# Performance work log

Measured on AMD Instinct MI355X. Metric: run time of the kernel, lower is better.

Reference implementation:

```python
import jax, jax.numpy as jnp
import numpy as np
import math

B, T, C, NH = 4, 2048, 1024, 16
D = C // NH  # 64, rotary_dim == D

def _rope_tables():
    inv_freq = 1.0 / (10000.0 ** (np.arange(0, D, 2, dtype=np.float32) / D))
    t = np.arange(T, dtype=np.float32)
    freqs = np.outer(t, inv_freq)                 # [T, D/2]
    emb = np.concatenate([freqs, freqs], axis=-1)  # [T, D]
    return jnp.asarray(np.cos(emb))[None], jnp.asarray(np.sin(emb))[None]  # [1,T,D]

def setup_inputs() -> dict:
    key = jax.random.key(0)
    ks = jax.random.split(key, 3)
    x = jax.random.normal(ks[0], (B, T, C), dtype=jnp.float32)
    w_attn = jax.random.normal(ks[1], (3 * C, C), dtype=jnp.float32) * (1.0 / math.sqrt(C))
    b_attn = jnp.zeros((3 * C,), dtype=jnp.float32)
    w_proj = jax.random.normal(ks[2], (C, C), dtype=jnp.float32) * (1.0 / math.sqrt(C))
    b_proj = jnp.zeros((C,), dtype=jnp.float32)
    cos, sin = _rope_tables()
    return {"x": x, "w_attn": w_attn, "b_attn": b_attn,
            "w_proj": w_proj, "b_proj": b_proj, "cos": cos, "sin": sin}

def _rotate_half(u):
    u1, u2 = jnp.split(u, 2, axis=-1)
    return jnp.concatenate([-u2, u1], axis=-1)

def reference(x, w_attn, b_attn, w_proj, b_proj, cos, sin):
    Bx, Tx, Cx = x.shape
    nh, d = NH, Cx // NH
    # fused QKV projection (torch Linear: y = x @ W^T + b)
    qkv = x @ w_attn.T + b_attn                      # [B,T,3C]
    q, k, v = jnp.split(qkv, 3, axis=-1)
    q = q.reshape(Bx, Tx, nh, d).transpose(0, 2, 1, 3)  # [B,nh,T,d]
    k = k.reshape(Bx, Tx, nh, d).transpose(0, 2, 1, 3)
    v = v.reshape(Bx, Tx, nh, d).transpose(0, 2, 1, 3)
    # RoPE (rotary_dim == d, full head)
    c = cos[:, None, :, :]  # [1,1,T,d]
    s = sin[:, None, :, :]
    q = q * c + _rotate_half(q) * s
    k = k * c + _rotate_half(k) * s
    # naive causal attention
    scores = jnp.einsum("bhqd,bhkd->bhqk", q, k) / math.sqrt(d)
    causal = jnp.tril(jnp.ones((Tx, Tx), dtype=bool))
    scores = jnp.where(causal[None, None], scores, -jnp.inf)
    att = jax.nn.softmax(scores, axis=-1)
    y = jnp.einsum("bhqk,bhkd->bhqd", att, v)        # [B,nh,T,d]
    y = y.transpose(0, 2, 1, 3).reshape(Bx, Tx, Cx)
    return y @ w_proj.T + b_proj
```

## Files before the change

### kernel.cpp

```cpp
#include <hip/hip_runtime.h>

typedef __bf16 bf16_t;
typedef bf16_t bf16x8 __attribute__((ext_vector_type(8)));
typedef bf16_t bf16x4 __attribute__((ext_vector_type(4)));
typedef float f32x4 __attribute__((ext_vector_type(4)));

constexpr int BATCH = 4, SEQ = 2048, CH = 1024, NHEAD = 16, HD = 64;
constexpr int BM = 128, BN = 128, BKK = 32;

#define LGKM_FENCE() __asm__ __volatile__("s_waitcnt lgkmcnt(0)" ::: "memory")
#define VM_FENCE() __asm__ __volatile__("s_waitcnt vmcnt(0)" ::: "memory")

__device__ __forceinline__ void g2lds16(const bf16_t* g, bf16_t* l) {
  __builtin_amdgcn_global_load_lds((__attribute__((address_space(1))) void*)(g),
                                   (__attribute__((address_space(3))) void*)(l),
                                   16, 0, 0);
}

__device__ __forceinline__ f32x4 mfma16(bf16x8 a, bf16x8 b, f32x4 c) {
  return __builtin_amdgcn_mfma_f32_16x16x32_bf16(a, b, c, 0, 0, 0);
}

__global__ __launch_bounds__(256) void cvt_kernel(const float4* __restrict__ src,
                                                  ushort4* __restrict__ dst, int n4) {
  int i = blockIdx.x * 256 + threadIdx.x;
  if (i >= n4) return;
  float4 f = src[i];
  ushort4 o;
  o.x = __builtin_bit_cast(unsigned short, (bf16_t)f.x);
  o.y = __builtin_bit_cast(unsigned short, (bf16_t)f.y);
  o.z = __builtin_bit_cast(unsigned short, (bf16_t)f.z);
  o.w = __builtin_bit_cast(unsigned short, (bf16_t)f.w);
  dst[i] = o;
}

__device__ __forceinline__ void gemm_mainloop(const bf16_t* __restrict__ A,
                                              const bf16_t* __restrict__ W, int Kdim,
                                              int m0, int n0,
                                              bf16_t* As, bf16_t* Bs,
                                              f32x4 acc[4][4]) {
  const int tid = threadIdx.x;
  const int lane = tid & 63, w = tid >> 6;
  const int quad = lane >> 4, l16 = lane & 15;
  const int wm = (w >> 1) << 6, wn = (w & 1) << 6;
  const int srow = (w << 5) + (lane >> 2);
  const int scol = (lane & 3) << 3;
  const bf16_t* ga0 = A + (size_t)(m0 + srow) * Kdim + scol;
  const bf16_t* ga1 = A + (size_t)(m0 + srow + 16) * Kdim + scol;
  const bf16_t* gb0 = W + (size_t)(n0 + srow) * Kdim + scol;
  const bf16_t* gb1 = W + (size_t)(n0 + srow + 16) * Kdim + scol;
  bf16_t* la0 = As + srow * BKK + scol;
  bf16_t* la1 = As + (srow + 16) * BKK + scol;
  bf16_t* lb0 = Bs + srow * BKK + scol;
  bf16_t* lb1 = Bs + (srow + 16) * BKK + scol;
  for (int k0 = 0; k0 < Kdim; k0 += BKK) {
    g2lds16(ga0 + k0, la0);
    g2lds16(ga1 + k0, la1);
    g2lds16(gb0 + k0, lb0);
    g2lds16(gb1 + k0, lb1);
    VM_FENCE();
    __syncthreads();
    bf16x8 av[4], bv[4];
#pragma unroll
    for (int i = 0; i < 4; i++)
      av[i] = *(const bf16x8*)&As[(wm + i * 16 + l16) * BKK + quad * 8];
#pragma unroll
    for (int i = 0; i < 4; i++)
      bv[i] = *(const bf16x8*)&Bs[(wn + i * 16 + l16) * BKK + quad * 8];
#pragma unroll
    for (int mi = 0; mi < 4; mi++)
#pragma unroll
      for (int ni = 0; ni < 4; ni++)
        acc[mi][ni] = mfma16(av[mi], bv[ni], acc[mi][ni]);
    __syncthreads();
  }
}

__global__ __launch_bounds__(256) void qkv_rope_kernel(
    const bf16_t* __restrict__ X, const bf16_t* __restrict__ Wa,
    const float* __restrict__ ba, const float* __restrict__ cosT,
    const float* __restrict__ sinT, bf16_t* __restrict__ Q,
    bf16_t* __restrict__ Ko, bf16_t* __restrict__ VT) {
  constexpr int TSTRIDE = 68;
  __shared__ __align__(16) char smem[4 * 64 * TSTRIDE * 2];
  bf16_t* As = (bf16_t*)smem;
  bf16_t* Bs = As + BM * BKK;

  f32x4 acc[4][4];
#pragma unroll
  for (int i = 0; i < 4; i++)
#pragma unroll
    for (int j = 0; j < 4; j++) acc[i][j] = (f32x4){0.f, 0.f, 0.f, 0.f};

  const int n0 = blockIdx.x * BN, m0 = blockIdx.y * BM;
  gemm_mainloop(X, Wa, CH, m0, n0, As, Bs, acc);

  const int tid = threadIdx.x, lane = tid & 63, w = tid >> 6;
  const int quad = lane >> 4, l16 = lane & 15;
  const int wm = (w >> 1) << 6, wn = (w & 1) << 6;
  const int nbase = n0 + wn;
  const int part = nbase >> 10;
  const int h = (nbase & 1023) >> 6;
  const int mbase = m0 + wm;
  const int bb = mbase >> 11;
  const size_t headbase = ((size_t)(bb * NHEAD + h)) * SEQ * HD;

  if (part < 2) {
    bf16_t* O = (part == 0) ? Q : Ko;
#pragma unroll
    for (int mi = 0; mi < 4; mi++)
#pragma unroll
      for (int r = 0; r < 4; r++) {
        int m = mbase + mi * 16 + quad * 4 + r;
        int t = m & (SEQ - 1);
        const float* cr = cosT + t * HD;
        const float* sr = sinT + t * HD;
        size_t rowo = headbase + (size_t)t * HD;
#pragma unroll
        for (int ni = 0; ni < 2; ni++) {
          int d0 = ni * 16 + l16, d1 = d0 + 32;
          float v0 = acc[mi][ni][r] + ba[nbase + d0];
          float v1 = acc[mi][ni + 2][r] + ba[nbase + d1];
          float r0 = v0 * cr[d0] - v1 * sr[d0];
          float r1 = v1 * cr[d1] + v0 * sr[d1];
          O[rowo + d0] = (bf16_t)r0;
          O[rowo + d1] = (bf16_t)r1;
        }
      }
  } else {
    bf16_t* tb = (bf16_t*)smem + w * 64 * TSTRIDE;
    int t0 = mbase & (SEQ - 1);
#pragma unroll
    for (int mi = 0; mi < 4; mi++)
#pragma unroll
      for (int ni = 0; ni < 4; ni++) {
        int d = ni * 16 + l16;
        float bias = ba[nbase + d];
#pragma unroll
        for (int r = 0; r < 4; r++) {
          float v = acc[mi][ni][r] + bias;
          tb[d * TSTRIDE + mi * 16 + quad * 4 + r] = (bf16_t)v;
        }
      }
    LGKM_FENCE();
    int half = lane >> 5, l5 = lane & 31;
    size_t vbase = ((size_t)(bb * NHEAD + h)) * HD * SEQ;
#pragma unroll
    for (int it = 0; it < 32; it++) {
      int d = it * 2 + half;
      unsigned int val = *(const unsigned int*)&tb[d * TSTRIDE + l5 * 2];
      *(unsigned int*)&VT[vbase + (size_t)d * SEQ + t0 + l5 * 2] = val;
    }
  }
}

constexpr int PS = 80;
constexpr float SCL = 0.125f * 1.44269504089f;

__device__ __forceinline__ void sm_update(f32x4 (&s)[4], float& mr, float& lr,
                                          f32x4 (&y)[4], bf16_t* Prow,
                                          bool domask, int lim) {
  if (domask) {
#pragma unroll
    for (int ni = 0; ni < 4; ni++)
#pragma unroll
      for (int r = 0; r < 4; r++)
        if (ni * 16 + r > lim) s[ni][r] = -1e30f;
  }
  f32x4 mx;
#pragma unroll
  for (int r = 0; r < 4; r++)
    mx[r] = fmaxf(fmaxf(s[0][r], s[1][r]), fmaxf(s[2][r], s[3][r]));
  float cm = fmaxf(fmaxf(mx[0], mx[1]), fmaxf(mx[2], mx[3]));
  cm = fmaxf(cm, __shfl_xor(cm, 16));
  cm = fmaxf(cm, __shfl_xor(cm, 32));
  float mn = fmaxf(mr, cm);
  float hof = -SCL * mn;
  float al = __builtin_exp2f(fmaf(mr, SCL, hof));
  mr = mn;
  float sum = 0.f;
#pragma unroll
  for (int ni = 0; ni < 4; ni++) {
    float p0 = __builtin_exp2f(fmaf(s[ni][0], SCL, hof));
    float p1 = __builtin_exp2f(fmaf(s[ni][1], SCL, hof));
    float p2 = __builtin_exp2f(fmaf(s[ni][2], SCL, hof));
    float p3 = __builtin_exp2f(fmaf(s[ni][3], SCL, hof));
    bf16x4 pk = {(bf16_t)p0, (bf16_t)p1, (bf16_t)p2, (bf16_t)p3};
    *(bf16x4*)&Prow[ni * 16] = pk;
    sum += (p0 + p1) + (p2 + p3);
  }
  lr = fmaf(lr, al, sum);
#pragma unroll
  for (int ni = 0; ni < 4; ni++) y[ni] *= al;
}

__global__ __launch_bounds__(256) void flash_kernel(const bf16_t* __restrict__ Q,
                                                    const bf16_t* __restrict__ Kg,
                                                    const bf16_t* __restrict__ VT,
                                                    bf16_t* __restrict__ att) {
  __shared__ __align__(16) bf16_t Ks[2][64 * 64];
  __shared__ __align__(16) bf16_t Vs[2][64 * 64];
  __shared__ __align__(16) bf16_t Pt[8][16 * PS];
  const int tid = threadIdx.x, w = tid >> 6, lane = tid & 63;
  const int quad = lane >> 4, l16 = lane & 15;
  const int bh = blockIdx.y;
  const bf16_t* Qp = Q + (size_t)bh * SEQ * HD;
  const bf16_t* Kb = Kg + (size_t)bh * SEQ * HD;
  const bf16_t* Vb = VT + (size_t)bh * HD * SEQ;
  const int grow = lane >> 3;
  const int gj8 = ((lane & 7) ^ grow) * 8;
  const int i0 = w * 2;
  const int sw = l16 & 7;
  const int bloc = bh >> 4, hh = bh & 15;
  bf16_t* PA = &Pt[w * 2 + 0][l16 * PS + quad * 4];
  bf16_t* PB = &Pt[w * 2 + 1][l16 * PS + quad * 4];
  const bf16_t* PAr = &Pt[w * 2 + 0][l16 * PS + quad * 8];
  const bf16_t* PBr = &Pt[w * 2 + 1][l16 * PS + quad * 8];

  auto stage = [&](int kcs, int b) {
#pragma unroll
    for (int ii = 0; ii < 2; ii++) {
      int i = i0 + ii;
      g2lds16(Kb + (size_t)(kcs + i * 8 + grow) * HD + gj8, &Ks[b][(i * 64 + lane) * 8]);
      g2lds16(Vb + (size_t)(i * 8 + grow) * SEQ + kcs + gj8, &Vs[b][(i * 64 + lane) * 8]);
    }
  };

  for (int sp = 0; sp < 2; ++sp) {
    const int qb = sp ? (int)blockIdx.x : 15 - (int)blockIdx.x;
    const int q0 = qb * 128;
    const int mA = q0 + w * 16, mB = mA + 64;
    bf16x8 aqA0 = *(const bf16x8*)&Qp[(size_t)(mA + l16) * HD + quad * 8];
    bf16x8 aqA1 = *(const bf16x8*)&Qp[(size_t)(mA + l16) * HD + 32 + quad * 8];
    bf16x8 aqB0 = *(const bf16x8*)&Qp[(size_t)(mB + l16) * HD + quad * 8];
    bf16x8 aqB1 = *(const bf16x8*)&Qp[(size_t)(mB + l16) * HD + 32 + quad * 8];
    float mrA = -1e30f, lrA = 0.f, mrB = -1e30f, lrB = 0.f;
    f32x4 yA[4], yB[4];
#pragma unroll
    for (int ni = 0; ni < 4; ni++) {
      yA[ni] = (f32x4){0.f, 0.f, 0.f, 0.f};
      yB[ni] = (f32x4){0.f, 0.f, 0.f, 0.f};
    }
    const int nch = 2 * qb + 2;

    stage(0, 0);
    VM_FENCE();
    __syncthreads();

    for (int c = 0; c < nch; ++c) {
      const int kc = c * 64, buf = c & 1;
      if (c + 1 < nch) stage(kc + 64, buf ^ 1);
      const bool doA = (c + 1 < nch);
      f32x4 sA[4], sB[4];
#pragma unroll
      for (int ni = 0; ni < 4; ni++) {
        bf16x8 k0 = *(const bf16x8*)&Ks[buf][((ni * 16 + l16) * 8 + (quad ^ sw)) * 8];
        bf16x8 k1 = *(const bf16x8*)&Ks[buf][((ni * 16 + l16) * 8 + ((4 + quad) ^ sw)) * 8];
        f32x4 z = (f32x4){0.f, 0.f, 0.f, 0.f};
        sB[ni] = mfma16(k1, aqB1, mfma16(k0, aqB0, z));
        if (doA) sA[ni] = mfma16(k1, aqA1, mfma16(k0, aqA0, z));
      }
      sm_update(sB, mrB, lrB, yB, PB, c == nch - 1, mB + l16 - kc - quad * 4);
      if (doA)
        sm_update(sA, mrA, lrA, yA, PA, c == nch - 2, mA + l16 - kc - quad * 4);
      LGKM_FENCE();
      bf16x8 pB0 = *(const bf16x8*)&PBr[0];
      bf16x8 pB1 = *(const bf16x8*)&PBr[32];
      bf16x8 pA0, pA1;
      if (doA) {
        pA0 = *(const bf16x8*)&PAr[0];
        pA1 = *(const bf16x8*)&PAr[32];
      }
#pragma unroll
      for (int ni = 0; ni < 4; ni++) {
        bf16x8 v0 = *(const bf16x8*)&Vs[buf][((ni * 16 + l16) * 8 + (quad ^ sw)) * 8];
        bf16x8 v1 = *(const bf16x8*)&Vs[buf][((ni * 16 + l16) * 8 + ((4 + quad) ^ sw)) * 8];
        yB[ni] = mfma16(v1, pB1, mfma16(v0, pB0, yB[ni]));
        if (doA) yA[ni] = mfma16(v1, pA1, mfma16(v0, pA0, yA[ni]));
      }
      VM_FENCE();
      __syncthreads();
    }

    lrA += __shfl_xor(lrA, 16);
    lrA += __shfl_xor(lrA, 32);
    lrB += __shfl_xor(lrB, 16);
    lrB += __shfl_xor(lrB, 32);
    float invA = 1.f / lrA, invB = 1.f / lrB;
    size_t rbA = ((size_t)bloc * SEQ + mA + l16) * CH + hh * HD + quad * 4;
    size_t rbB = ((size_t)bloc * SEQ + mB + l16) * CH + hh * HD + quad * 4;
#pragma unroll
    for (int ni = 0; ni < 4; ni++) {
      bf16x4 oA = {(bf16_t)(yA[ni][0] * invA), (bf16_t)(yA[ni][1] * invA),
                   (bf16_t)(yA[ni][2] * invA), (bf16_t)(yA[ni][3] * invA)};
      bf16x4 oB = {(bf16_t)(yB[ni][0] * invB), (bf16_t)(yB[ni][1] * invB),
                   (bf16_t)(yB[ni][2] * invB), (bf16_t)(yB[ni][3] * invB)};
      *(bf16x4*)&att[rbA + ni * 16] = oA;
      *(bf16x4*)&att[rbB + ni * 16] = oB;
    }
  }
}

__global__ __launch_bounds__(256) void proj_kernel(const bf16_t* __restrict__ A,
                                                   const bf16_t* __restrict__ Wp,
                                                   const float* __restrict__ bp,
                                                   float* __restrict__ out) {
  __shared__ __align__(16) bf16_t As[BM * BKK];
  __shared__ __align__(16) bf16_t Bs[BN * BKK];
  f32x4 acc[4][4];
#pragma unroll
  for (int i = 0; i < 4; i++)
#pragma unroll
    for (int j = 0; j < 4; j++) acc[i][j] = (f32x4){0.f, 0.f, 0.f, 0.f};
  const int n0 = blockIdx.x * BN, m0 = blockIdx.y * BM;
  gemm_mainloop(A, Wp, CH, m0, n0, As, Bs, acc);
  const int tid = threadIdx.x, lane = tid & 63, w = tid >> 6;
  const int quad = lane >> 4, l16 = lane & 15;
  const int wm = (w >> 1) << 6, wn = (w & 1) << 6;
  const int nbase = n0 + wn, mbase = m0 + wm;
#pragma unroll
  for (int mi = 0; mi < 4; mi++)
#pragma unroll
    for (int r = 0; r < 4; r++) {
      int m = mbase + mi * 16 + quad * 4 + r;
#pragma unroll
      for (int ni = 0; ni < 4; ni++) {
        int n = nbase + ni * 16 + l16;
        out[(size_t)m * CH + n] = acc[mi][ni][r] + bp[n];
      }
    }
}

extern "C" void kernel_launch(void* const* d_in, const int* in_sizes, int n_in,
                              void* d_out, int out_size, void* d_ws, size_t ws_size,
                              hipStream_t stream) {
  const float* x      = (const float*)d_in[0];
  const float* w_attn = (const float*)d_in[1];
  const float* b_attn = (const float*)d_in[2];
  const float* w_proj = (const float*)d_in[3];
  const float* b_proj = (const float*)d_in[4];
  const float* cosT   = (const float*)d_in[5];
  const float* sinT   = (const float*)d_in[6];
  float* out = (float*)d_out;

  bf16_t* xbf  = (bf16_t*)d_ws;
  bf16_t* wabf = xbf + (size_t)8192 * 1024;
  bf16_t* wpbf = wabf + (size_t)3072 * 1024;
  bf16_t* Qb   = wpbf + (size_t)1024 * 1024;
  bf16_t* Kb   = Qb + (size_t)8388608;
  bf16_t* VTb  = Kb + (size_t)8388608;
  bf16_t* attb = VTb + (size_t)8388608;

  cvt_kernel<<<8192, 256, 0, stream>>>((const float4*)x, (ushort4*)xbf, 2097152);
  cvt_kernel<<<3072, 256, 0, stream>>>((const float4*)w_attn, (ushort4*)wabf, 786432);
  cvt_kernel<<<1024, 256, 0, stream>>>((const float4*)w_proj, (ushort4*)wpbf, 262144);
  qkv_rope_kernel<<<dim3(24, 64), 256, 0, stream>>>(xbf, wabf, b_attn, cosT, sinT,
                                                    Qb, Kb, VTb);
  flash_kernel<<<dim3(8, 64), 256, 0, stream>>>(Qb, Kb, VTb, attb);
  proj_kernel<<<dim3(8, 64), 256, 0, stream>>>(attb, wpbf, b_proj, out);
}
```

Before: 310.7 us.

## Restructure flash attention grid, fold softmax scale into Q, lazy rescale

Folds the softmax scale and log2e factor into Q inside the QKV/RoPE epilogue, so the flash kernel computes exp2(s - m) directly. Online-softmax rescaling of the accumulator is skipped when no row max grows in the wave. The flash grid changes from 8x64 blocks that each process two query blocks to 1024 one-dimensional blocks, one query block each, ordered heaviest-first. The P staging buffer shrinks to one XOR-swizzled tile per wave with occupancy hinted at 4 blocks/CU, and V fragments are preloaded and reused by both row halves. Risks are more blocks with uneven causal work and the extra precision loss from rounding the pre-scaled Q to bf16.

```diff
diff --git a/kernel.cpp b/kernel.cpp
--- a/kernel.cpp
+++ b/kernel.cpp
@@ -10,6 +10,7 @@
 
 #define LGKM_FENCE() __asm__ __volatile__("s_waitcnt lgkmcnt(0)" ::: "memory")
 #define VM_FENCE() __asm__ __volatile__("s_waitcnt vmcnt(0)" ::: "memory")
+#define REORDER_FENCE() __asm__ __volatile__("" ::: "memory")
 
 __device__ __forceinline__ void g2lds16(const bf16_t* g, bf16_t* l) {
   __builtin_amdgcn_global_load_lds((__attribute__((address_space(1))) void*)(g),
@@ -76,6 +77,8 @@
   }
 }
 
+constexpr float SCL = 0.125f * 1.44269504089f;
+
 __global__ __launch_bounds__(256) void qkv_rope_kernel(
     const bf16_t* __restrict__ X, const bf16_t* __restrict__ Wa,
     const float* __restrict__ ba, const float* __restrict__ cosT,
@@ -107,6 +110,7 @@
 
   if (part < 2) {
     bf16_t* O = (part == 0) ? Q : Ko;
+    const float post = (part == 0) ? SCL : 1.0f;
 #pragma unroll
     for (int mi = 0; mi < 4; mi++)
 #pragma unroll
@@ -121,8 +125,8 @@
           int d0 = ni * 16 + l16, d1 = d0 + 32;
           float v0 = acc[mi][ni][r] + ba[nbase + d0];
           float v1 = acc[mi][ni + 2][r] + ba[nbase + d1];
-          float r0 = v0 * cr[d0] - v1 * sr[d0];
-          float r1 = v1 * cr[d1] + v0 * sr[d1];
+          float r0 = (v0 * cr[d0] - v1 * sr[d0]) * post;
+          float r1 = (v1 * cr[d1] + v0 * sr[d1]) * post;
           O[rowo + d0] = (bf16_t)r0;
           O[rowo + d1] = (bf16_t)r1;
         }
@@ -154,11 +158,8 @@
   }
 }
 
-constexpr int PS = 80;
-constexpr float SCL = 0.125f * 1.44269504089f;
-
 __device__ __forceinline__ void sm_update(f32x4 (&s)[4], float& mr, float& lr,
-                                          f32x4 (&y)[4], bf16_t* Prow,
+                                          f32x4 (&y)[4], bf16_t* Prow, int xk,
                                           bool domask, int lim) {
   if (domask) {
 #pragma unroll
@@ -174,36 +175,39 @@
   float cm = fmaxf(fmaxf(mx[0], mx[1]), fmaxf(mx[2], mx[3]));
   cm = fmaxf(cm, __shfl_xor(cm, 16));
   cm = fmaxf(cm, __shfl_xor(cm, 32));
-  float mn = fmaxf(mr, cm);
-  float hof = -SCL * mn;
-  float al = __builtin_exp2f(fmaf(mr, SCL, hof));
-  mr = mn;
+  if (__any(cm > mr)) {
+    float mn = fmaxf(mr, cm);
+    float al = __builtin_exp2f(mr - mn);
+    mr = mn;
+    lr *= al;
+#pragma unroll
+    for (int ni = 0; ni < 4; ni++) y[ni] *= al;
+  }
   float sum = 0.f;
 #pragma unroll
   for (int ni = 0; ni < 4; ni++) {
-    float p0 = __builtin_exp2f(fmaf(s[ni][0], SCL, hof));
-    float p1 = __builtin_exp2f(fmaf(s[ni][1], SCL, hof));
-    float p2 = __builtin_exp2f(fmaf(s[ni][2], SCL, hof));
-    float p3 = __builtin_exp2f(fmaf(s[ni][3], SCL, hof));
+    float p0 = __builtin_exp2f(s[ni][0] - mr);
+    float p1 = __builtin_exp2f(s[ni][1] - mr);
+    float p2 = __builtin_exp2f(s[ni][2] - mr);
+    float p3 = __builtin_exp2f(s[ni][3] - mr);
     bf16x4 pk = {(bf16_t)p0, (bf16_t)p1, (bf16_t)p2, (bf16_t)p3};
-    *(bf16x4*)&Prow[ni * 16] = pk;
+    *(bf16x4*)&Prow[((ni ^ xk) << 4)] = pk;
     sum += (p0 + p1) + (p2 + p3);
   }
-  lr = fmaf(lr, al, sum);
-#pragma unroll
-  for (int ni = 0; ni < 4; ni++) y[ni] *= al;
-}
-
-__global__ __launch_bounds__(256) void flash_kernel(const bf16_t* __restrict__ Q,
-                                                    const bf16_t* __restrict__ Kg,
-                                                    const bf16_t* __restrict__ VT,
-                                                    bf16_t* __restrict__ att) {
+  lr += sum;
+}
+
+__global__ __launch_bounds__(256, 4) void flash_kernel(const bf16_t* __restrict__ Q,
+                                                       const bf16_t* __restrict__ Kg,
+                                                       const bf16_t* __restrict__ VT,
+                                                       bf16_t* __restrict__ att) {
   __shared__ __align__(16) bf16_t Ks[2][64 * 64];
   __shared__ __align__(16) bf16_t Vs[2][64 * 64];
-  __shared__ __align__(16) bf16_t Pt[8][16 * PS];
+  __shared__ __align__(16) bf16_t Pt[4][16 * 64];
   const int tid = threadIdx.x, w = tid >> 6, lane = tid & 63;
   const int quad = lane >> 4, l16 = lane & 15;
-  const int bh = blockIdx.y;
+  const int qb = 15 - ((int)blockIdx.x >> 6);
+  const int bh = (int)blockIdx.x & 63;
   const bf16_t* Qp = Q + (size_t)bh * SEQ * HD;
   const bf16_t* Kb = Kg + (size_t)bh * SEQ * HD;
   const bf16_t* Vb = VT + (size_t)bh * HD * SEQ;
@@ -211,11 +215,12 @@
   const int gj8 = ((lane & 7) ^ grow) * 8;
   const int i0 = w * 2;
   const int sw = l16 & 7;
+  const int xk = l16 & 3;
   const int bloc = bh >> 4, hh = bh & 15;
-  bf16_t* PA = &Pt[w * 2 + 0][l16 * PS + quad * 4];
-  bf16_t* PB = &Pt[w * 2 + 1][l16 * PS + quad * 4];
-  const bf16_t* PAr = &Pt[w * 2 + 0][l16 * PS + quad * 8];
-  const bf16_t* PBr = &Pt[w * 2 + 1][l16 * PS + quad * 8];
+  bf16_t* Pw = &Pt[w][l16 * 64];
+  bf16_t* Pwr = Pw + quad * 4;
+  const int rs0 = ((2 * quad) ^ (xk << 2)) << 2;
+  const int rs1 = ((8 + 2 * quad) ^ (xk << 2)) << 2;
 
   auto stage = [&](int kcs, int b) {
 #pragma unroll
@@ -226,78 +231,77 @@
     }
   };
 
-  for (int sp = 0; sp < 2; ++sp) {
-    const int qb = sp ? (int)blockIdx.x : 15 - (int)blockIdx.x;
-    const int q0 = qb * 128;
-    const int mA = q0 + w * 16, mB = mA + 64;
-    bf16x8 aqA0 = *(const bf16x8*)&Qp[(size_t)(mA + l16) * HD + quad * 8];
-    bf16x8 aqA1 = *(const bf16x8*)&Qp[(size_t)(mA + l16) * HD + 32 + quad * 8];
-    bf16x8 aqB0 = *(const bf16x8*)&Qp[(size_t)(mB + l16) * HD + quad * 8];
-    bf16x8 aqB1 = *(const bf16x8*)&Qp[(size_t)(mB + l16) * HD + 32 + quad * 8];
-    float mrA = -1e30f, lrA = 0.f, mrB = -1e30f, lrB = 0.f;
-    f32x4 yA[4], yB[4];
+  const int q0 = qb * 128;
+  const int mA = q0 + w * 16, mB = mA + 64;
+  bf16x8 aqA0 = *(const bf16x8*)&Qp[(size_t)(mA + l16) * HD + quad * 8];
+  bf16x8 aqA1 = *(const bf16x8*)&Qp[(size_t)(mA + l16) * HD + 32 + quad * 8];
+  bf16x8 aqB0 = *(const bf16x8*)&Qp[(size_t)(mB + l16) * HD + quad * 8];
+  bf16x8 aqB1 = *(const bf16x8*)&Qp[(size_t)(mB + l16) * HD + 32 + quad * 8];
+  float mrA = -1e30f, lrA = 0.f, mrB = -1e30f, lrB = 0.f;
+  f32x4 yA[4], yB[4];
+#pragma unroll
+  for (int ni = 0; ni < 4; ni++) {
+    yA[ni] = (f32x4){0.f, 0.f, 0.f, 0.f};
+    yB[ni] = (f32x4){0.f, 0.f, 0.f, 0.f};
+  }
+  const int nch = 2 * qb + 2;
+
+  stage(0, 0);
+  VM_FENCE();
+  __syncthreads();
+
+  for (int c = 0; c < nch; ++c) {
+    const int kc = c * 64, buf = c & 1;
+    if (c + 1 < nch) stage(kc + 64, buf ^ 1);
+    const bool doA = (c + 1 < nch);
+    f32x4 sA[4], sB[4];
+    bf16x8 vf0[4], vf1[4];
 #pragma unroll
     for (int ni = 0; ni < 4; ni++) {
-      yA[ni] = (f32x4){0.f, 0.f, 0.f, 0.f};
-      yB[ni] = (f32x4){0.f, 0.f, 0.f, 0.f};
-    }
-    const int nch = 2 * qb + 2;
-
-    stage(0, 0);
+      bf16x8 k0 = *(const bf16x8*)&Ks[buf][((ni * 16 + l16) * 8 + (quad ^ sw)) * 8];
+      bf16x8 k1 = *(const bf16x8*)&Ks[buf][((ni * 16 + l16) * 8 + ((4 + quad) ^ sw)) * 8];
+      f32x4 z = (f32x4){0.f, 0.f, 0.f, 0.f};
+      sB[ni] = mfma16(k1, aqB1, mfma16(k0, aqB0, z));
+      if (doA) sA[ni] = mfma16(k1, aqA1, mfma16(k0, aqA0, z));
+      vf0[ni] = *(const bf16x8*)&Vs[buf][((ni * 16 + l16) * 8 + (quad ^ sw)) * 8];
+      vf1[ni] = *(const bf16x8*)&Vs[buf][((ni * 16 + l16) * 8 + ((4 + quad) ^ sw)) * 8];
+    }
+    sm_update(sB, mrB, lrB, yB, Pwr, xk, c == nch - 1, mB + l16 - kc - quad * 4);
+    LGKM_FENCE();
+    bf16x8 pB0 = *(const bf16x8*)&Pw[rs0];
+    bf16x8 pB1 = *(const bf16x8*)&Pw[rs1];
+#pragma unroll
+    for (int ni = 0; ni < 4; ni++)
+      yB[ni] = mfma16(vf1[ni], pB1, mfma16(vf0[ni], pB0, yB[ni]));
+    if (doA) {
+      REORDER_FENCE();
+      sm_update(sA, mrA, lrA, yA, Pwr, xk, c == nch - 2, mA + l16 - kc - quad * 4);
+      LGKM_FENCE();
+      bf16x8 pA0 = *(const bf16x8*)&Pw[rs0];
+      bf16x8 pA1 = *(const bf16x8*)&Pw[rs1];
+#pragma unroll
+      for (int ni = 0; ni < 4; ni++)
+        yA[ni] = mfma16(vf1[ni], pA1, mfma16(vf0[ni], pA0, yA[ni]));
+    }
     VM_FENCE();
     __syncthreads();
-
-    for (int c = 0; c < nch; ++c) {
-      const int kc = c * 64, buf = c & 1;
-      if (c + 1 < nch) stage(kc + 64, buf ^ 1);
-      const bool doA = (c + 1 < nch);
-      f32x4 sA[4], sB[4];
-#pragma unroll
-      for (int ni = 0; ni < 4; ni++) {
-        bf16x8 k0 = *(const bf16x8*)&Ks[buf][((ni * 16 + l16) * 8 + (quad ^ sw)) * 8];
-        bf16x8 k1 = *(const bf16x8*)&Ks[buf][((ni * 16 + l16) * 8 + ((4 + quad) ^ sw)) * 8];
-        f32x4 z = (f32x4){0.f, 0.f, 0.f, 0.f};
-        sB[ni] = mfma16(k1, aqB1, mfma16(k0, aqB0, z));
-        if (doA) sA[ni] = mfma16(k1, aqA1, mfma16(k0, aqA0, z));
-      }
-      sm_update(sB, mrB, lrB, yB, PB, c == nch - 1, mB + l16 - kc - quad * 4);
-      if (doA)
-        sm_update(sA, mrA, lrA, yA, PA, c == nch - 2, mA + l16 - kc - quad * 4);
-      LGKM_FENCE();
-      bf16x8 pB0 = *(const bf16x8*)&PBr[0];
-      bf16x8 pB1 = *(const bf16x8*)&PBr[32];
-      bf16x8 pA0, pA1;
-      if (doA) {
-        pA0 = *(const bf16x8*)&PAr[0];
-        pA1 = *(const bf16x8*)&PAr[32];
-      }
-#pragma unroll
-      for (int ni = 0; ni < 4; ni++) {
-        bf16x8 v0 = *(const bf16x8*)&Vs[buf][((ni * 16 + l16) * 8 + (quad ^ sw)) * 8];
-        bf16x8 v1 = *(const bf16x8*)&Vs[buf][((ni * 16 + l16) * 8 + ((4 + quad) ^ sw)) * 8];
-        yB[ni] = mfma16(v1, pB1, mfma16(v0, pB0, yB[ni]));
-        if (doA) yA[ni] = mfma16(v1, pA1, mfma16(v0, pA0, yA[ni]));
-      }
-      VM_FENCE();
-      __syncthreads();
-    }
-
-    lrA += __shfl_xor(lrA, 16);
-    lrA += __shfl_xor(lrA, 32);
-    lrB += __shfl_xor(lrB, 16);
-    lrB += __shfl_xor(lrB, 32);
-    float invA = 1.f / lrA, invB = 1.f / lrB;
-    size_t rbA = ((size_t)bloc * SEQ + mA + l16) * CH + hh * HD + quad * 4;
-    size_t rbB = ((size_t)bloc * SEQ + mB + l16) * CH + hh * HD + quad * 4;
-#pragma unroll
-    for (int ni = 0; ni < 4; ni++) {
-      bf16x4 oA = {(bf16_t)(yA[ni][0] * invA), (bf16_t)(yA[ni][1] * invA),
-                   (bf16_t)(yA[ni][2] * invA), (bf16_t)(yA[ni][3] * invA)};
-      bf16x4 oB = {(bf16_t)(yB[ni][0] * invB), (bf16_t)(yB[ni][1] * invB),
-                   (bf16_t)(yB[ni][2] * invB), (bf16_t)(yB[ni][3] * invB)};
-      *(bf16x4*)&att[rbA + ni * 16] = oA;
-      *(bf16x4*)&att[rbB + ni * 16] = oB;
-    }
+  }
+
+  lrA += __shfl_xor(lrA, 16);
+  lrA += __shfl_xor(lrA, 32);
+  lrB += __shfl_xor(lrB, 16);
+  lrB += __shfl_xor(lrB, 32);
+  float invA = 1.f / lrA, invB = 1.f / lrB;
+  size_t rbA = ((size_t)bloc * SEQ + mA + l16) * CH + hh * HD + quad * 4;
+  size_t rbB = ((size_t)bloc * SEQ + mB + l16) * CH + hh * HD + quad * 4;
+#pragma unroll
+  for (int ni = 0; ni < 4; ni++) {
+    bf16x4 oA = {(bf16_t)(yA[ni][0] * invA), (bf16_t)(yA[ni][1] * invA),
+                 (bf16_t)(yA[ni][2] * invA), (bf16_t)(yA[ni][3] * invA)};
+    bf16x4 oB = {(bf16_t)(yB[ni][0] * invB), (bf16_t)(yB[ni][1] * invB),
+                 (bf16_t)(yB[ni][2] * invB), (bf16_t)(yB[ni][3] * invB)};
+    *(bf16x4*)&att[rbA + ni * 16] = oA;
+    *(bf16x4*)&att[rbB + ni * 16] = oB;
   }
 }
 
@@ -356,6 +360,6 @@
   cvt_kernel<<<1024, 256, 0, stream>>>((const float4*)w_proj, (ushort4*)wpbf, 262144);
   qkv_rope_kernel<<<dim3(24, 64), 256, 0, stream>>>(xbf, wabf, b_attn, cosT, sinT,
                                                     Qb, Kb, VTb);
-  flash_kernel<<<dim3(8, 64), 256, 0, stream>>>(Qb, Kb, VTb, attb);
+  flash_kernel<<<dim3(1024), 256, 0, stream>>>(Qb, Kb, VTb, attb);
   proj_kernel<<<dim3(8, 64), 256, 0, stream>>>(attb, wpbf, b_proj, out);
 }
```

Measured after the change: 480.8 us. 54.7% more time.
